# Optimization experiments

Measured on AMD Instinct MI355X. Metric: run time of the kernel, lower is better.

The kernel has to match this reference:

```python
import jax, jax.numpy as jnp
from jax import lax
import numpy as np

B, A, T = 128, 32, 32
HID = 64
DEG = 7
MODES = 25
OUT_FRAMES = 12
NHEAD, DHEAD = 16, 64


def legendre_tmat(out_frames, degree):
    # normalized Legendre basis evaluated at t_n, shape [degree+1, len(t_n)]
    t = np.arange(-6, out_frames + 1, dtype=np.float32)
    t = t / t[-1]
    P = [np.ones_like(t), t]
    for n in range(1, degree):
        P.append(((2 * n + 1) * t * P[n] - n * P[n - 1]) / (n + 1))
    P = np.stack(P[: degree + 1], 0)
    norm = np.sqrt((2 * np.arange(degree + 1) + 1) / 2.0).astype(np.float32)
    return (P * norm[:, None]).astype(np.float32)


def _conv(x, w, stride, pad):
    return lax.conv_general_dilated(x, w, (stride, stride), [(pad, pad), (pad, pad)],
                                    dimension_numbers=("NCHW", "OIHW", "NCHW"))


def _bn(x, g, b, eps=1e-5):
    m = jnp.mean(x, axis=(0, 2, 3), keepdims=True)
    v = jnp.var(x, axis=(0, 2, 3), keepdims=True)
    return (x - m) / jnp.sqrt(v + eps) * g[None, :, None, None] + b[None, :, None, None]


def setup_inputs() -> dict:
    key = jax.random.key(0)
    ks = jax.random.split(key, 32)

    def rn(i, shape, scale=0.05):
        return jax.random.normal(ks[i], shape, dtype=jnp.float32) * scale

    inp = {
        "cnn_feat": rn(0, (B, 1024, 14, 14), 1.0),
        "ego_state": rn(1, (B, T, 5), 1.0),
        "agents_state": rn(2, (B, A, T, 5), 1.0),
        "ego_state_len": jax.random.randint(ks[3], (B,), 0, T),
        "agents_state_len": jax.random.randint(ks[4], (B, A), 0, T),
        "agents_grid_pos": jax.random.randint(ks[5], (B, A, 2), 0, 14),
        "state_fc_W": rn(6, (HID, 5)), "state_fc_b": rn(7, (HID,)),
        "lstm_Wih": rn(8, (4 * HID, HID)), "lstm_Whh": rn(9, (4 * HID, HID)),
        "lstm_bih": rn(10, (4 * HID,)), "lstm_bhh": rn(11, (4 * HID,)),
        "enc_fc_W": rn(12, (HID, HID)), "enc_fc_b": rn(13, (HID,)),
        "conv1_W": rn(14, (512, 1024 + HID, 3, 3)),
        "bn1_g": jnp.ones((512,), jnp.float32), "bn1_b": jnp.zeros((512,), jnp.float32),
        "conv2_W": rn(15, (512, 512, 3, 3)),
        "bn2_g": jnp.ones((512,), jnp.float32), "bn2_b": jnp.zeros((512,), jnp.float32),
        "q_W": rn(16, (NHEAD * DHEAD, 512 + HID)),
        "k_W": rn(17, (NHEAD * DHEAD, 512, 1, 1)),
        "v_W": rn(18, (NHEAD * DHEAD, 512, 1, 1)),
        "attn_out_W": rn(19, (512, NHEAD * DHEAD)), "attn_out_b": rn(20, (512,)),
        "cls_W": rn(21, (MODES, 512 + HID + 512)), "cls_b": rn(22, (MODES,)),
        "dec1_W": rn(23, (256, 512 + HID + 512)), "dec1_b": rn(24, (256,)),
        "dec2_W": rn(25, ((DEG + 1) * 2 * MODES, 256)), "dec2_b": rn(26, ((DEG + 1) * 2 * MODES,)),
    }
    return inp


def reference(cnn_feat, ego_state, agents_state, ego_state_len, agents_state_len,
              agents_grid_pos, state_fc_W, state_fc_b, lstm_Wih, lstm_Whh, lstm_bih,
              lstm_bhh, enc_fc_W, enc_fc_b, conv1_W, bn1_g, bn1_b, conv2_W, bn2_g,
              bn2_b, q_W, k_W, v_W, attn_out_W, attn_out_b, cls_W, cls_b, dec1_W,
              dec1_b, dec2_W, dec2_b):
    Bn, _, Hs, Ws = cnn_feat.shape

    def lstm_encode(seq, lens):
        # seq [N,T,5]; packed-sequence semantics with zero init == take h at step len-1
        N, Tn, _ = seq.shape
        h = seq @ state_fc_W.T + state_fc_b  # [N,T,64]

        def step(carry, xt):
            hh, cc = carry
            g = xt @ lstm_Wih.T + hh @ lstm_Whh.T + lstm_bih + lstm_bhh
            i, f_, gg, o = jnp.split(g, 4, axis=-1)
            cc = jax.nn.sigmoid(f_) * cc + jax.nn.sigmoid(i) * jnp.tanh(gg)
            hh = jax.nn.sigmoid(o) * jnp.tanh(cc)
            return (hh, cc), hh

        z = jnp.zeros((N, HID), h.dtype)
        _, hs = lax.scan(step, (z, z), h.transpose(1, 0, 2))  # hs [T,N,64]
        idx = jnp.clip(lens, 1, Tn).astype(jnp.int32) - 1
        last = hs[idx, jnp.arange(N)]
        return last @ enc_fc_W.T + enc_fc_b

    ego = lstm_encode(ego_state, ego_state_len)  # [B,64]
    ag = lstm_encode(agents_state.reshape(Bn * A, T, 5),
                     agents_state_len.reshape(-1)).reshape(Bn, A, HID)

    # scatter-add agent encodings into the spatial grid (overlapping writes accumulate)
    grid = jnp.zeros((Bn, Hs, Ws, HID), cnn_feat.dtype)
    bidx = jnp.broadcast_to(jnp.arange(Bn)[:, None], (Bn, A))
    grid = grid.at[bidx, agents_grid_pos[..., 0], agents_grid_pos[..., 1]].add(ag)

    x = jnp.concatenate([cnn_feat, grid.transpose(0, 3, 1, 2)], axis=1)
    x = jax.nn.relu(_bn(_conv(x, conv1_W, 1, 1), bn1_g, bn1_b))
    x = jax.nn.relu(_bn(_conv(x, conv2_W, 2, 1), bn2_g, bn2_b))  # [B,512,7,7]

    ego_t = jnp.concatenate([x[:, :, 3, 3], ego], axis=1)  # [B,576]
    q = (ego_t @ q_W.T).reshape(Bn, NHEAD, DHEAD)
    k = _conv(x, k_W, 1, 1).reshape(Bn, NHEAD, DHEAD, -1)  # g = 9*9 = 81
    v = _conv(x, v_W, 1, 1).reshape(Bn, NHEAD, DHEAD, -1)
    energy = jnp.einsum("bhf,bhfg->bhg", q, k)
    attn = jax.nn.softmax(energy / (NHEAD * DHEAD) ** 0.5, axis=2)
    o = jnp.einsum("bhg,bhdg->bhd", attn, v).reshape(Bn, -1)
    o = o @ attn_out_W.T + attn_out_b

    feat = jnp.concatenate([o, ego_t], axis=1)  # [B,1088]
    conf = feat @ cls_W.T + cls_b
    d = jax.nn.relu(feat @ dec1_W.T + dec1_b)
    d = (d @ dec2_W.T + dec2_b).reshape(Bn, MODES, -1)

    tmat = jnp.asarray(legendre_tmat(OUT_FRAMES, DEG))  # [DEG+1, 19]
    out_x = d[:, :, : DEG + 1] @ tmat
    out_y = d[:, :, DEG + 1:] @ tmat
    traj = jnp.stack([out_x, out_y], axis=3)  # [B,MODES,19,2]
    return traj, conf
```

## Files before the change

kernel.cpp:

```cpp
#include <hip/hip_runtime.h>
#include <stdint.h>
#include <stddef.h>

#define DEVINL static __device__ __forceinline__

typedef __attribute__((ext_vector_type(8))) short  bfrag;
typedef __attribute__((ext_vector_type(4))) float  facc;

DEVINL uint16_t f2b(float f){
  uint32_t u = __float_as_uint(f);
  return (uint16_t)((u + 0x7fffu + ((u >> 16) & 1u)) >> 16);
}
DEVINL float b2f(uint16_t b){ return __uint_as_float(((uint32_t)b) << 16); }

DEVINL facc MFMA(bfrag a, bfrag b, facc c){
  return __builtin_amdgcn_mfma_f32_16x16x32_bf16(a, b, c, 0, 0, 0);
}

DEVINL void gload16(const void* g, void* l){
  __builtin_amdgcn_global_load_lds(
      (const __attribute__((address_space(1))) uint32_t*)g,
      (__attribute__((address_space(3))) uint32_t*)l, 16, 0, 0);
}

DEVINL float fast_tanh(float x){
  return 2.f/(1.f+__expf(-2.f*x)) - 1.f;
}

struct F2BJobs {
  const float* s[6];
  uint16_t*    d[6];
  int          n[6];
};
__global__ void k_f2b_multi(F2BJobs jobs){
  int j = blockIdx.y;
  const float* s = jobs.s[j];
  uint16_t* d = jobs.d[j];
  int n = jobs.n[j];
  int i = blockIdx.x*256 + threadIdx.x;
  int st = gridDim.x*256;
  for(; i<n; i+=st) d[i] = f2b(s[i]);
}

__global__ void k_zborder(uint16_t* __restrict__ X, uint16_t* __restrict__ Y,
                          float* __restrict__ gridb){
  int b = blockIdx.x & 127, t = threadIdx.x;
  uint16_t* base = (blockIdx.x < 128) ? X : Y;
  int C = (blockIdx.x < 128) ? 1088 : 512;
  for(int p=0;p<60;p++){
    int y, x;
    if(p<16){ y=0; x=p; }
    else if(p<32){ y=15; x=p-16; }
    else { int q=p-32; y=1+(q>>1); x=(q&1)?15:0; }
    uint32_t* dst = (uint32_t*)(base + ((size_t)(b*16+y)*16 + x)*C);
    for(int i=t;i<C/2;i+=256) dst[i] = 0;
  }
  float* g = gridb + (size_t)blockIdx.x*6272;
  for(int i=t;i<6272;i+=256) g[i] = 0.f;
}

__global__ void k_lstm_prep(const float* __restrict__ Wih, const float* __restrict__ Whh,
                            const float* __restrict__ bih, const float* __restrict__ bhh,
                            const float* __restrict__ sW, const float* __restrict__ sb,
                            const float* __restrict__ encW,
                            uint16_t* __restrict__ Wc, float* __restrict__ be,
                            uint16_t* __restrict__ encWb, float* __restrict__ tm){
  int n = threadIdx.x;
  if(n < 19){
    float tv = (float)(n - 6) / 12.0f;
    float Pm = 1.0f, Pc = tv;
    tm[0*19+n] = Pm * sqrtf(0.5f);
    tm[1*19+n] = Pc * sqrtf(1.5f);
    for(int q=1; q<7; q++){
      float Pn = ((float)(2*q+1)*tv*Pc - (float)q*Pm) / (float)(q+1);
      Pm = Pc; Pc = Pn;
      tm[(q+1)*19+n] = Pc * sqrtf((float)(2*(q+1)+1) * 0.5f);
    }
  }
  for(int k=0;k<64;k++) Wc[n*96+k] = f2b(Whh[n*64+k]);
  for(int k5=0;k5<5;k5++){
    float s = 0.f;
    for(int j=0;j<64;j++) s += Wih[n*64+j]*sW[j*5+k5];
    Wc[n*96+64+k5] = f2b(s);
  }
  for(int k=69;k<96;k++) Wc[n*96+k] = 0;
  float s = 0.f;
  for(int j=0;j<64;j++) s += Wih[n*64+j]*sb[j];
  be[n] = s + bih[n] + bhh[n];
  if(n < 64){
    for(int k=0;k<64;k++) encWb[n*64+k] = f2b(encW[n*64+k]);
  }
}

__global__ __launch_bounds__(256) void k_lstm(
    const float* __restrict__ ego_seq, const float* __restrict__ ag_seq,
    const int* __restrict__ ego_len, const int* __restrict__ ag_len,
    const int* __restrict__ grid_pos,
    const uint16_t* __restrict__ Wc, const float* __restrict__ be,
    const uint16_t* __restrict__ encWb, const float* __restrict__ encB,
    float* __restrict__ agrid, uint16_t* __restrict__ egoT, uint16_t* __restrict__ feat)
{
  __shared__ __align__(16) uint16_t A[32*96];
  __shared__ float Xf[32*160];
  __shared__ int   idxs[32];

  int t = threadIdx.x, w = t>>6, l = t&63;
  int blk = blockIdx.x;
  bool isEgo = blk < 4;
  int seq0 = isEgo ? blk*32 : (blk-4)*32;
  const float* seqp = (isEgo ? ego_seq : ag_seq) + (size_t)seq0*160;

  for(int i=t;i<32*160;i+=256) Xf[i] = seqp[i];
  if(t < 32){
    int L = isEgo ? ego_len[seq0+t] : ag_len[seq0+t];
    if(L < 1) L = 1;
    idxs[t] = L-1;
  }
  for(int i=t;i<32*96;i+=256) A[i] = 0;

  bfrag bf[4][3];
  float be4[4];
  for(int ct=0;ct<4;ct++){
    int n = (ct*4+w)*16 + (l&15);
    for(int ks=0;ks<3;ks++)
      bf[ct][ks] = *(const bfrag*)(Wc + n*96 + ks*32 + (l>>4)*8);
    be4[ct] = be[n];
  }
  float cst[8], hl[8];
  for(int i=0;i<8;i++){ cst[i]=0.f; hl[i]=0.f; }
  __syncthreads();
  int myidx[8];
  for(int rt=0;rt<2;rt++) for(int r=0;r<4;r++){
    int s = rt*16 + (l>>4)*4 + r;
    myidx[rt*4+r] = idxs[s];
  }

  for(int st=0; st<32; st++){
    if(t < 160){ int s=t/5, kk=t%5; A[s*96+64+kk] = f2b(Xf[s*160 + st*5 + kk]); }
    __syncthreads();
    facc acc[2][4];
    for(int rt=0;rt<2;rt++) for(int ct=0;ct<4;ct++) acc[rt][ct] = facc{0.f,0.f,0.f,0.f};
    #pragma unroll
    for(int ks=0;ks<3;ks++){
      bfrag aA[2];
      #pragma unroll
      for(int rt=0;rt<2;rt++)
        aA[rt] = *(const bfrag*)(A + (rt*16+(l&15))*96 + ks*32 + (l>>4)*8);
      #pragma unroll
      for(int rt=0;rt<2;rt++)
        #pragma unroll
        for(int ct=0;ct<4;ct++)
          acc[rt][ct] = MFMA(aA[rt], bf[ct][ks], acc[rt][ct]);
    }
    __syncthreads();
    #pragma unroll
    for(int rt=0;rt<2;rt++) for(int r=0;r<4;r++){
      int cell = rt*4+r;
      int s = rt*16 + (l>>4)*4 + r;
      float gi = acc[rt][0][r] + be4[0];
      float gf = acc[rt][1][r] + be4[1];
      float gg = acc[rt][2][r] + be4[2];
      float go = acc[rt][3][r] + be4[3];
      float si = 1.f/(1.f+__expf(-gi));
      float sf = 1.f/(1.f+__expf(-gf));
      float so = 1.f/(1.f+__expf(-go));
      float tg = fast_tanh(gg);
      float c2 = sf*cst[cell] + si*tg;
      cst[cell] = c2;
      float hn = so*fast_tanh(c2);
      A[s*96 + w*16 + (l&15)] = f2b(hn);
      if(st == myidx[cell]) hl[cell] = hn;
    }
  }
  __syncthreads();
  for(int rt=0;rt<2;rt++) for(int r=0;r<4;r++){
    int s = rt*16 + (l>>4)*4 + r;
    A[s*96 + w*16 + (l&15)] = f2b(hl[rt*4+r]);
  }
  __syncthreads();
  bfrag eb[2];
  for(int ks=0;ks<2;ks++)
    eb[ks] = *(const bfrag*)(encWb + (w*16+(l&15))*64 + ks*32 + (l>>4)*8);
  facc ea[2]; ea[0] = facc{0.f,0.f,0.f,0.f}; ea[1] = facc{0.f,0.f,0.f,0.f};
  for(int ks=0;ks<2;ks++){
    for(int rt=0;rt<2;rt++){
      bfrag aA = *(const bfrag*)(A + (rt*16+(l&15))*96 + ks*32 + (l>>4)*8);
      ea[rt] = MFMA(aA, eb[ks], ea[rt]);
    }
  }
  int n = w*16 + (l&15);
  float bn_ = encB[n];
  for(int rt=0;rt<2;rt++) for(int r=0;r<4;r++){
    int s = rt*16 + (l>>4)*4 + r;
    float v = ea[rt][r] + bn_;
    int gs = seq0 + s;
    if(isEgo){
      egoT[(size_t)gs*576 + 512 + n] = f2b(v);
      feat[(size_t)gs*1088 + 1024 + n] = f2b(v);
    } else {
      int py = grid_pos[gs*2+0], px = grid_pos[gs*2+1];
      atomicAdd(&agrid[((size_t)(gs>>5)*196 + py*14 + px)*64 + n], v);
    }
  }
}

__global__ void k_packx(const float* __restrict__ cnn, const float* __restrict__ agrid,
                        uint16_t* __restrict__ Xp)
{
  __shared__ float tile[32*200];
  int b = blockIdx.x, ch = blockIdx.y, t = threadIdx.x;
  if(ch < 32){
    int c0 = ch*32;
    for(int i=t;i<32*196;i+=256){
      int ci = i/196, s = i%196;
      tile[ci*200+s] = cnn[((size_t)b*1024 + c0+ci)*196 + s];
    }
    __syncthreads();
    for(int i=t;i<16*196;i+=256){
      int s = i>>4, c2 = i&15;
      int y = s/14, x = s%14;
      uint32_t pu = (uint32_t)f2b(tile[(2*c2)*200+s]) |
                    ((uint32_t)f2b(tile[(2*c2+1)*200+s])<<16);
      *(uint32_t*)(Xp + (((size_t)b*16 + y+1)*16 + x+1)*1088 + c0 + 2*c2) = pu;
    }
  } else {
    int j0 = (ch-32)*32;
    for(int i=t;i<16*196;i+=256){
      int s = i>>4, j2 = i&15;
      int y = s/14, x = s%14;
      const float* gsrc = agrid + ((size_t)b*196 + s)*64 + j0 + 2*j2;
      uint32_t pu = (uint32_t)f2b(gsrc[0]) | ((uint32_t)f2b(gsrc[1])<<16);
      *(uint32_t*)(Xp + (((size_t)b*16 + y+1)*16 + x+1)*1088 + 1024 + j0 + 2*j2) = pu;
    }
  }
}

__global__ void k_packw(const float* __restrict__ W, uint16_t* __restrict__ Wp, int O, int C)
{
  int o = blockIdx.x;
  int c = blockIdx.y*64 + threadIdx.x;
  const float* src = W + ((size_t)o*C + c)*9;
  float v[9];
  #pragma unroll
  for(int d=0;d<9;d++) v[d] = src[d];
  #pragma unroll
  for(int d=0;d<9;d++)
    Wp[((size_t)d*O + o)*C + c] = f2b(v[d]);
}

__global__ void k_packw2(const float* __restrict__ W, uint16_t* __restrict__ Wp)
{
  int o = blockIdx.x;
  int c = blockIdx.y*64 + threadIdx.x;
  const float* src = W + ((size_t)o*512 + c)*9;
  float v[9];
  #pragma unroll
  for(int d=0;d<9;d++) v[d] = src[d];
  #pragma unroll
  for(int dy=0;dy<3;dy++)
    #pragma unroll
    for(int dx=0;dx<3;dx++)
      Wp[((size_t)(dy*512 + o))*1536 + dx*512 + c] = f2b(v[dy*3+dx]);
}

__global__ void k_packwk(const float* __restrict__ kW, uint16_t* __restrict__ WKT)
{
  int h = blockIdx.x;
  int c0 = blockIdx.y*32;
  int t = threadIdx.x;
  int d = t & 63;
  for(int ci = t>>6; ci<32; ci+=4){
    int c = c0 + ci;
    WKT[((size_t)h*512 + c)*64 + d] = f2b(kW[((size_t)(h*64+d))*512 + c]);
  }
}

__global__ __launch_bounds__(512) void k_conv1_8p(
    const uint16_t* __restrict__ Ain, const uint16_t* __restrict__ Wb,
    uint16_t* __restrict__ Out, float* __restrict__ stats)
{
  constexpr int CB = 1088;
  constexpr int NSTEP = 153;
  __shared__ __align__(16) char LDSb[131072];

  int t = threadIdx.x, w = t>>6, l = t&63;
  int wm = w>>2, wn = w&3;

  int xcd = blockIdx.x & 7, pos = blockIdx.x >> 3;
  int wgid = (xcd < 4 ? xcd*25 : 100 + (xcd-4)*24) + pos;
  int m0 = (wgid % 98) * 256;
  int n0 = (wgid / 98) * 256;

  const uint16_t* aP[2][2];
  const uint16_t* bP[2][2];
  #pragma unroll
  for(int P=0;P<2;P++)
    #pragma unroll
    for(int j=0;j<2;j++){
      int partrow = j*64 + (t>>3);
      int swz = ((t&7) ^ (partrow&7))*8;
      int gr = P*64 + partrow + ((partrow>=64)?64:0);
      int m = m0 + gr; int b = m/196, s = m%196, y = s/14, x = s%14;
      aP[P][j] = Ain + ((b*16+y)*16+x)*CB + swz;
      int nb = n0 + (partrow>>5)*64 + P*32 + (partrow&31);
      bP[P][j] = Wb + (size_t)nb*CB + swz;
    }

  facc acc[8][4];
  #pragma unroll
  for(int i=0;i<8;i++)
    #pragma unroll
    for(int j=0;j<4;j++) acc[i][j] = facc{0.f,0.f,0.f,0.f};

  bfrag aF[4][2], bF0[2][2], bF1[2][2];
  int dd = 0;

  #define STG(buf, PART) do{                                                   \
    if((PART)==0 || (PART)==3){ const int P_ = ((PART)==3);                    \
      _Pragma("unroll")                                                        \
      for(int j_=0;j_<2;j_++)                                                  \
        gload16(aP[P_][j_], LDSb + (buf)*65536 + P_*16384 + j_*8192 + w*1024); \
    } else { const int P_ = ((PART)==2);                                       \
      _Pragma("unroll")                                                        \
      for(int j_=0;j_<2;j_++)                                                  \
        gload16(bP[P_][j_], LDSb + (buf)*65536 + 32768 + P_*16384 + j_*8192 + w*1024); \
    }                                                                          \
  }while(0)

  #define ADVK() do{                                                          \
    if(dd==8){                                                                \
      _Pragma("unroll")                                                       \
      for(int P_=0;P_<2;P_++) for(int j_=0;j_<2;j_++){                        \
        aP[P_][j_] += 64 - 34*CB; bP[P_][j_] += 64 - 8*512*CB; }              \
      dd = 0;                                                                 \
    } else {                                                                  \
      int sA_ = (dd==2||dd==5) ? 14*CB : CB;                                  \
      _Pragma("unroll")                                                       \
      for(int P_=0;P_<2;P_++) for(int j_=0;j_<2;j_++){                        \
        aP[P_][j_] += sA_; bP[P_][j_] += 512*CB; }                            \
      dd++;                                                                   \
    }                                                                         \
  }while(0)

  #define VM4 asm volatile("s_waitcnt vmcnt(4)" ::: "memory")
  #define VM2 asm volatile("s_waitcnt vmcnt(2)" ::: "memory")
  #define VM0 asm volatile("s_waitcnt vmcnt(0)" ::: "memory")

  #define LDA(mh) do{                                                         \
    const uint16_t* Ab_ = (const uint16_t*)(LDSb + p*65536 + (mh)*16384);     \
    _Pragma("unroll")                                                         \
    for(int i_=0;i_<4;i_++)                                                   \
      _Pragma("unroll")                                                       \
      for(int ks_=0;ks_<2;ks_++)                                              \
        aF[i_][ks_] = *(const bfrag*)(Ab_ + (wm*64 + i_*16 + (l&15))*64       \
                        + ((ks_*32 + (l>>4)*8) ^ ((l&7)<<3)));                \
  }while(0)

  #define LDB(dst, nh) do{                                                   \
    const uint16_t* Bb_ = (const uint16_t*)(LDSb + p*65536 + 32768 + (nh)*16384); \
    _Pragma("unroll")                                                         \
    for(int j_=0;j_<2;j_++)                                                   \
      _Pragma("unroll")                                                       \
      for(int ks_=0;ks_<2;ks_++)                                              \
        dst[j_][ks_] = *(const bfrag*)(Bb_ + (wn*32 + j_*16 + (l&15))*64      \
                        + ((ks_*32 + (l>>4)*8) ^ ((l&7)<<3)));                \
  }while(0)

  #define MM(mh, nh, bsrc) do{                                               \
    __builtin_amdgcn_s_setprio(1);                                           \
    _Pragma("unroll")                                                        \
    for(int ks_=0;ks_<2;ks_++)                                               \
      _Pragma("unroll")                                                      \
      for(int i_=0;i_<4;i_++)                                                \
        _Pragma("unroll")                                                    \
        for(int j_=0;j_<2;j_++)                                              \
          acc[(mh)*4+i_][(nh)*2+j_] =                                        \
            MFMA(aF[i_][ks_], bsrc[j_][ks_], acc[(mh)*4+i_][(nh)*2+j_]);     \
    __builtin_amdgcn_s_setprio(0);                                           \
  }while(0)

  #define BARS do{ __builtin_amdgcn_sched_barrier(0); __builtin_amdgcn_s_barrier(); }while(0)
  #define EBAR __builtin_amdgcn_s_barrier()

  STG(0,0); STG(0,1); STG(0,2); STG(0,3);
  ADVK();
  VM4;
  EBAR;

  for(int kt=0; kt<NSTEP-1; kt++){
    int p = kt&1;
    LDA(0); LDB(bF0,0); STG(p^1,0); BARS; MM(0,0,bF0); VM4; EBAR;
    LDB(bF1,1);         STG(p^1,1); BARS; MM(0,1,bF1); VM4; EBAR;
    LDA(1);             STG(p^1,2); BARS; MM(1,1,bF1);      EBAR;
                        STG(p^1,3); BARS; MM(1,0,bF0); VM4; EBAR;
    if(kt < NSTEP-2) ADVK();
  }
  {
    int p = 0;
    LDA(0); LDB(bF0,0); BARS; MM(0,0,bF0); VM2; EBAR;
    LDB(bF1,1);         BARS; MM(0,1,bF1); VM0; EBAR;
    LDA(1);             BARS; MM(1,1,bF1);      EBAR;
                        BARS; MM(1,0,bF0);      EBAR;
  }

  #undef LDA
  #undef LDB
  #undef MM
  #undef BARS
  #undef EBAR
  #undef STG
  #undef ADVK

  __syncthreads();
  int* oo = (int*)LDSb;
  if(t < 256){
    int m = m0 + t; int b = m/196, s = m%196, y = s/14, x = s%14;
    oo[t] = ((b*16 + y+1)*16 + (x+1))*512;
  }
  __syncthreads();
  #pragma unroll
  for(int i=0;i<8;i++)
    #pragma unroll
    for(int j=0;j<4;j++){
      int n = n0 + wn*64 + j*16 + (l&15);
      #pragma unroll
      for(int r=0;r<4;r++){
        int mr = wm*128 + i*16 + (l>>4)*4 + r;
        Out[(size_t)oo[mr] + n] = f2b(acc[i][j][r]);
      }
    }
  __syncthreads();
  float* sred = (float*)LDSb;
  int rg = wm*4 + (l>>4);
  #pragma unroll
  for(int j=0;j<4;j++){
    float s=0.f, q=0.f;
    #pragma unroll
    for(int i=0;i<8;i++)
      #pragma unroll
      for(int r=0;r<4;r++){ float v = acc[i][j][r]; s += v; q += v*v; }
    int nl = wn*64 + j*16 + (l&15);
    sred[(nl*8 + rg)*2+0] = s;
    sred[(nl*8 + rg)*2+1] = q;
  }
  __syncthreads();
  if(t < 256){
    float s=0.f, q=0.f;
    #pragma unroll
    for(int rgi=0;rgi<8;rgi++){ s += sred[(t*8+rgi)*2]; q += sred[(t*8+rgi)*2+1]; }
    atomicAdd(&stats[n0+t], s);
    atomicAdd(&stats[512+n0+t], q);
  }
}

__global__ __launch_bounds__(256) void k_conv2dy(
    const uint16_t* __restrict__ Ain, const uint16_t* __restrict__ Wb,
    uint16_t* __restrict__ PS)
{
  __shared__ __align__(16) uint16_t As[128*64];
  __shared__ __align__(16) uint16_t Bs[128*64];

  int t = threadIdx.x, w = t>>6, l = t&63;
  int dy = blockIdx.y;

  int xcd = blockIdx.x & 7, pos = blockIdx.x >> 3;
  int wgid = (xcd < 4 ? xcd*25 : 100 + (xcd-4)*24) + pos;
  int n0 = (wgid / 49) * 128;
  int m0 = (wgid % 49) * 128;

  const uint16_t* aP[4];
  const uint16_t* bP[4];
  #pragma unroll
  for(int p=0;p<4;p++){
    int r = w*32 + p*8 + (l>>3);
    int m = m0 + r;
    int b = m/49, s = m%49, y = s/7, x = s%7;
    aP[p] = Ain + ((b*16 + 2*y + dy)*16 + 2*x)*512 + (l&7)*8;
    bP[p] = Wb + ((size_t)(dy*512 + n0 + r))*1536 + (l&7)*8;
  }

  facc acc[4][4];
  #pragma unroll
  for(int i=0;i<4;i++)
    #pragma unroll
    for(int j=0;j<4;j++) acc[i][j] = facc{0.f,0.f,0.f,0.f};
  int wm = w>>1, wn = w&1;
  char* asDst = (char*)As + w*4096;
  char* bsDst = (char*)Bs + w*4096;

  for(int stp=0; stp<24; stp++){
    #pragma unroll
    for(int p=0;p<4;p++){ gload16(aP[p], asDst + p*1024); aP[p] += 64; }
    #pragma unroll
    for(int p=0;p<4;p++){ gload16(bP[p], bsDst + p*1024); bP[p] += 64; }
    __syncthreads();
    #pragma unroll
    for(int ks=0;ks<2;ks++){
      bfrag a[4], b[4];
      #pragma unroll
      for(int i=0;i<4;i++)
        a[i] = *(const bfrag*)(As + (wm*64 + i*16 + (l&15))*64 + ks*32 + (l>>4)*8);
      #pragma unroll
      for(int j=0;j<4;j++)
        b[j] = *(const bfrag*)(Bs + (wn*64 + j*16 + (l&15))*64 + ks*32 + (l>>4)*8);
      #pragma unroll
      for(int i=0;i<4;i++)
        #pragma unroll
        for(int j=0;j<4;j++)
          acc[i][j] = MFMA(a[i], b[j], acc[i][j]);
    }
    __syncthreads();
  }

  uint16_t* out = PS + (size_t)dy*3211264;
  #pragma unroll
  for(int i=0;i<4;i++)
    #pragma unroll
    for(int j=0;j<4;j++){
      int n = n0 + wn*64 + j*16 + (l&15);
      #pragma unroll
      for(int r=0;r<4;r++){
        int mr = m0 + wm*64 + i*16 + (l>>4)*4 + r;
        out[(size_t)mr*512 + n] = f2b(acc[i][j][r]);
      }
    }
}

__global__ void k_bn2sum(const uint16_t* __restrict__ PS, uint16_t* __restrict__ Y2,
                         float* __restrict__ stats)
{
  int t = threadIdx.x;
  int m0 = blockIdx.x*16;
  float s0=0,s1=0,q0=0,q1=0;
  for(int i=0;i<16;i++){
    size_t off = (size_t)(m0+i)*512 + 2*t;
    uint32_t u0 = *(const uint32_t*)(PS + off);
    uint32_t u1 = *(const uint32_t*)(PS + 3211264 + off);
    uint32_t u2 = *(const uint32_t*)(PS + 6422528 + off);
    float a = b2f((uint16_t)u0)+b2f((uint16_t)u1)+b2f((uint16_t)u2);
    float c = b2f((uint16_t)(u0>>16))+b2f((uint16_t)(u1>>16))+b2f((uint16_t)(u2>>16));
    s0+=a; q0+=a*a; s1+=c; q1+=c*c;
    *(uint32_t*)(Y2 + off) = (uint32_t)f2b(a) | ((uint32_t)f2b(c)<<16);
  }
  atomicAdd(&stats[2*t],   s0);
  atomicAdd(&stats[2*t+1], s1);
  atomicAdd(&stats[512+2*t],   q0);
  atomicAdd(&stats[512+2*t+1], q1);
}

template<int PAD>
__global__ void k_bnapply(uint16_t* __restrict__ Y, const float* __restrict__ stats,
                          const float* __restrict__ gg, const float* __restrict__ bb,
                          int M, float invM,
                          uint16_t* __restrict__ egoT, uint16_t* __restrict__ feat)
{
  int t = threadIdx.x;
  int m0 = blockIdx.x*8;
  float mu0 = stats[2*t]*invM,       mu1 = stats[2*t+1]*invM;
  float v0 = stats[512+2*t]*invM - mu0*mu0, v1 = stats[512+2*t+1]*invM - mu1*mu1;
  float sc0 = gg[2*t]  *rsqrtf(v0+1e-5f), sc1 = gg[2*t+1]*rsqrtf(v1+1e-5f);
  float sh0 = bb[2*t]   - mu0*sc0,        sh1 = bb[2*t+1] - mu1*sc1;
  for(int i=0;i<8;i++){
    int m = m0+i; if(m>=M) break;
    size_t off;
    if(PAD){ int b=m/196, s=m%196, y=s/14, x=s%14; off = (((size_t)b*16+y+1)*16 + x+1)*512; }
    else off = (size_t)m*512;
    uint32_t u = *(const uint32_t*)(Y + off + 2*t);
    float a = fmaxf(b2f((uint16_t)u)*sc0 + sh0, 0.f);
    float c = fmaxf(b2f((uint16_t)(u>>16))*sc1 + sh1, 0.f);
    uint32_t pu = (uint32_t)f2b(a) | ((uint32_t)f2b(c)<<16);
    *(uint32_t*)(Y + off + 2*t) = pu;
    if(!PAD && (m%49)==24){
      int b = m/49;
      *(uint32_t*)(egoT + (size_t)b*576 + 2*t) = pu;
      *(uint32_t*)(feat + (size_t)b*1088 + 512 + 2*t) = pu;
    }
  }
}

__global__ __launch_bounds__(256) void k_sgemm(
    const uint16_t* __restrict__ A, int lda,
    const uint16_t* __restrict__ B, int ldb,
    const float* __restrict__ bias,
    void* __restrict__ C, int ldc,
    int N, int K, int flags)
{
  int t = threadIdx.x, w = t>>6, l = t&63;
  int nt = blockIdx.x*4 + w;
  int n  = nt*16 + (l&15);
  int m0 = blockIdx.y*16;
  bool nv = n < N;
  facc acc = facc{0.f,0.f,0.f,0.f};
  for(int k=0;k<K;k+=32){
    bfrag af = *(const bfrag*)(A + (size_t)(m0+(l&15))*lda + k + (l>>4)*8);
    bfrag bf_ = {0,0,0,0,0,0,0,0};
    if(nv) bf_ = *(const bfrag*)(B + (size_t)n*ldb + k + (l>>4)*8);
    acc = MFMA(af, bf_, acc);
  }
  if(nv){
    float bv = bias ? bias[n] : 0.f;
    #pragma unroll
    for(int r=0;r<4;r++){
      int m = m0 + (l>>4)*4 + r;
      float v = acc[r] + bv;
      if(flags & 1) v = fmaxf(v, 0.f);
      if(flags & 2) ((float*)C)[(size_t)m*ldc + n] = v;
      else ((uint16_t*)C)[(size_t)m*ldc + n] = f2b(v);
    }
  }
}

__global__ __launch_bounds__(256) void k_bgemm(
    const uint16_t* __restrict__ A, int lda, int aoffs,
    const uint16_t* __restrict__ B, int ldb, int brows,
    uint16_t* __restrict__ C, int ldc, int coffs,
    int K)
{
  int t = threadIdx.x, w = t>>6, l = t&63;
  int z = blockIdx.z;
  int n = (blockIdx.x*4 + w)*16 + (l&15);
  int m0 = blockIdx.y*16;
  const uint16_t* Ab = A + (size_t)z*aoffs;
  const uint16_t* Bb = B + (size_t)z*brows*ldb;
  facc acc = facc{0.f,0.f,0.f,0.f};
  for(int k=0;k<K;k+=32){
    bfrag af = *(const bfrag*)(Ab + (size_t)(m0+(l&15))*lda + k + (l>>4)*8);
    bfrag bf_ = *(const bfrag*)(Bb + (size_t)n*ldb + k + (l>>4)*8);
    acc = MFMA(af, bf_, acc);
  }
  #pragma unroll
  for(int r=0;r<4;r++){
    int m = m0 + (l>>4)*4 + r;
    C[(size_t)m*ldc + z*coffs + n] = f2b(acc[r]);
  }
}

__global__ __launch_bounds__(512) void k_attn2(
    const uint16_t* __restrict__ U16, const uint16_t* __restrict__ y2,
    uint16_t* __restrict__ zout)
{
  __shared__ __align__(16) char LA[49*1024 + 8*1024];
  uint16_t* uls = (uint16_t*)(LA + 49*1024);
  int t = threadIdx.x, w = t>>6, l = t&63;
  int b = blockIdx.x >> 1, half = blockIdx.x & 1;
  int h = half*8 + w;

  for(int i=t; i<3136; i+=512){
    int g = i>>6, c16 = i&63;
    *(uint4*)(LA + g*1024 + ((c16*16) ^ ((g&31)<<4))) =
        *(const uint4*)(y2 + ((size_t)(b*49+g)*512 + c16*8));
  }
  *(uint4*)((char*)uls + w*1024 + l*16) =
      *(const uint4*)(U16 + (size_t)b*8192 + h*512 + l*8);
  __syncthreads();

  float dot = 0.f;
  if(l < 49){
    const char* yrow = LA + l*1024;
    const char* ur = (const char*)uls + w*1024;
    for(int c16=0;c16<64;c16++){
      uint4 uv = *(const uint4*)(ur + c16*16);
      uint4 yv = *(const uint4*)(yrow + ((c16*16) ^ ((l&31)<<4)));
      const uint16_t* up = (const uint16_t*)&uv;
      const uint16_t* yp = (const uint16_t*)&yv;
      #pragma unroll
      for(int j=0;j<8;j++) dot += b2f(up[j])*b2f(yp[j]);
    }
  }
  float e = (l<49) ? dot*(1.f/32.f) : -1e30f;
  float mx = e;
  for(int s=32;s>0;s>>=1) mx = fmaxf(mx, __shfl_xor(mx, s));
  mx = fmaxf(mx, 0.f);
  float p = (l<49) ? __expf(e-mx) : 0.f;
  float den = p;
  for(int s=32;s>0;s>>=1) den += __shfl_xor(den, s);
  den += 32.f*__expf(-mx);

  float z[8];
  #pragma unroll
  for(int j=0;j<8;j++) z[j]=0.f;
  for(int g=0; g<49; g++){
    float pg = __shfl(p, g);
    uint4 yv = *(const uint4*)(LA + g*1024 + ((l*16) ^ ((g&31)<<4)));
    const uint16_t* yp = (const uint16_t*)&yv;
    #pragma unroll
    for(int j=0;j<8;j++) z[j] += pg*b2f(yp[j]);
  }
  float inv = 1.f/den;
  uint16_t zr[8];
  #pragma unroll
  for(int j=0;j<8;j++) zr[j] = f2b(z[j]*inv);
  *(uint4*)(zout + ((size_t)(b*16+h)*512) + l*8) = *(uint4*)zr;
}

__global__ void k_traj(const float* __restrict__ d2, const float* __restrict__ tm,
                       float* __restrict__ out)
{
  int i = blockIdx.x*256 + threadIdx.x;
  if(i >= 3200) return;
  const float* dp = d2 + (size_t)i*16;
  float cx[8], cy[8];
  #pragma unroll
  for(int j=0;j<8;j++){ cx[j]=dp[j]; cy[j]=dp[8+j]; }
  float* op = out + (size_t)i*38;
  for(int tt=0;tt<19;tt++){
    float x=0.f, y=0.f;
    #pragma unroll
    for(int j=0;j<8;j++){ float tv = tm[j*19+tt]; x += cx[j]*tv; y += cy[j]*tv; }
    op[tt*2+0]=x; op[tt*2+1]=y;
  }
}

extern "C" void kernel_launch(void* const* d_in, const int* in_sizes, int n_in,
                              void* d_out, int out_size, void* d_ws, size_t ws_size,
                              hipStream_t stream)
{
  const float* cnn      = (const float*)d_in[0];
  const float* ego_seq  = (const float*)d_in[1];
  const float* ag_seq   = (const float*)d_in[2];
  const int*   ego_len  = (const int*)d_in[3];
  const int*   ag_len   = (const int*)d_in[4];
  const int*   grid_pos = (const int*)d_in[5];
  const float* sW  = (const float*)d_in[6];
  const float* sb  = (const float*)d_in[7];
  const float* Wih = (const float*)d_in[8];
  const float* Whh = (const float*)d_in[9];
  const float* bih = (const float*)d_in[10];
  const float* bhh = (const float*)d_in[11];
  const float* encW = (const float*)d_in[12];
  const float* encB = (const float*)d_in[13];
  const float* conv1W = (const float*)d_in[14];
  const float* bn1g = (const float*)d_in[15];
  const float* bn1b = (const float*)d_in[16];
  const float* conv2W = (const float*)d_in[17];
  const float* bn2g = (const float*)d_in[18];
  const float* bn2b = (const float*)d_in[19];
  const float* qWf  = (const float*)d_in[20];
  const float* kWf  = (const float*)d_in[21];
  const float* vWf  = (const float*)d_in[22];
  const float* aoW  = (const float*)d_in[23];
  const float* aoB  = (const float*)d_in[24];
  const float* clsWf = (const float*)d_in[25];
  const float* clsB  = (const float*)d_in[26];
  const float* d1Wf  = (const float*)d_in[27];
  const float* d1B   = (const float*)d_in[28];
  const float* d2Wf  = (const float*)d_in[29];
  const float* d2B   = (const float*)d_in[30];

  char* ws = (char*)d_ws;
  const size_t XP_OFF   = 0;
  const size_t PS_OFF   = 0;
  const size_t U_OFF    = 0;
  const size_t ZB_OFF   = 2097152;
  const size_t Y2_OFF   = 41943040;
  const size_t Y1P_OFF  = 71303168;
  const size_t WP1_OFF  = 104857600;
  const size_t WP2_OFF  = 114884608;
  const size_t WKT_OFF  = 119603200;
  const size_t WVB_OFF  = 120651776;
  const size_t QW_OFF   = 121700352;
  const size_t AOW_OFF  = 122880000;
  const size_t CLSW_OFF = 123928576;
  const size_t D1W_OFF  = 123982976;
  const size_t D2W_OFF  = 124540032;
  const size_t GRID_OFF = 124744832;
  const size_t EGOT_OFF = 131167360;
  const size_t FEAT_OFF = 131314816;
  const size_t QB_OFF   = 131593344;
  const size_t OBUF_OFF = 132117632;
  const size_t D1_OFF   = 132379776;
  const size_t D2_OFF   = 132445312;
  const size_t WC_OFF   = 132650112;
  const size_t BE_OFF   = 132699264;
  const size_t ENCW_OFF = 132700288;
  const size_t TMAT_OFF = 132708480;
  const size_t ST1_OFF  = 132709120;
  const size_t ST2_OFF  = 132713216;

  uint16_t* XP   = (uint16_t*)(ws + XP_OFF);
  uint16_t* PSB  = (uint16_t*)(ws + PS_OFF);
  uint16_t* U16  = (uint16_t*)(ws + U_OFF);
  uint16_t* ZB16 = (uint16_t*)(ws + ZB_OFF);
  uint16_t* Y2   = (uint16_t*)(ws + Y2_OFF);
  uint16_t* Y1P  = (uint16_t*)(ws + Y1P_OFF);
  uint16_t* WP1  = (uint16_t*)(ws + WP1_OFF);
  uint16_t* WP2  = (uint16_t*)(ws + WP2_OFF);
  uint16_t* WKT  = (uint16_t*)(ws + WKT_OFF);
  uint16_t* WVB  = (uint16_t*)(ws + WVB_OFF);
  uint16_t* QW   = (uint16_t*)(ws + QW_OFF);
  uint16_t* AOW  = (uint16_t*)(ws + AOW_OFF);
  uint16_t* CLSW = (uint16_t*)(ws + CLSW_OFF);
  uint16_t* D1W  = (uint16_t*)(ws + D1W_OFF);
  uint16_t* D2W  = (uint16_t*)(ws + D2W_OFF);
  float*    GRIDB= (float*)(ws + GRID_OFF);
  uint16_t* EGOT = (uint16_t*)(ws + EGOT_OFF);
  uint16_t* FEAT = (uint16_t*)(ws + FEAT_OFF);
  uint16_t* QB16 = (uint16_t*)(ws + QB_OFF);
  uint16_t* OBUF = (uint16_t*)(ws + OBUF_OFF);
  uint16_t* D1B  = (uint16_t*)(ws + D1_OFF);
  float*    D2B  = (float*)(ws + D2_OFF);
  uint16_t* WC   = (uint16_t*)(ws + WC_OFF);
  float*    BE   = (float*)(ws + BE_OFF);
  uint16_t* ENCWB= (uint16_t*)(ws + ENCW_OFF);
  float*    TMAT = (float*)(ws + TMAT_OFF);
  float*    ST1  = (float*)(ws + ST1_OFF);
  float*    ST2  = (float*)(ws + ST2_OFF);
  float*    outF = (float*)d_out;

  (void)hipMemsetAsync(ws + ST1_OFF,  0, 8192, stream);

  k_zborder<<<256,256,0,stream>>>(XP, Y1P, GRIDB);

  k_lstm_prep<<<1,256,0,stream>>>(Wih,Whh,bih,bhh,sW,sb,encW, WC,BE,ENCWB, TMAT);
  k_packw<<<dim3(512,17),64,0,stream>>>(conv1W, WP1, 512, 1088);
  k_packw2<<<dim3(512,8),64,0,stream>>>(conv2W, WP2);
  k_packwk<<<dim3(16,16),256,0,stream>>>(kWf, WKT);
  {
    F2BJobs jb;
    jb.s[0]=vWf;  jb.d[0]=WVB;   jb.n[0]=1024*512;
    jb.s[1]=qWf;  jb.d[1]=QW;    jb.n[1]=1024*576;
    jb.s[2]=aoW;  jb.d[2]=AOW;   jb.n[2]=512*1024;
    jb.s[3]=clsWf;jb.d[3]=CLSW;  jb.n[3]=25*1088;
    jb.s[4]=d1Wf; jb.d[4]=D1W;   jb.n[4]=256*1088;
    jb.s[5]=d2Wf; jb.d[5]=D2W;   jb.n[5]=400*256;
    k_f2b_multi<<<dim3(48,6),256,0,stream>>>(jb);
  }

  k_lstm<<<132,256,0,stream>>>(ego_seq, ag_seq, ego_len, ag_len, grid_pos,
                               WC, BE, ENCWB, encB, GRIDB, EGOT, FEAT);
  k_packx<<<dim3(128,34),256,0,stream>>>(cnn, GRIDB, XP);
  k_conv1_8p<<<196,512,0,stream>>>(XP, WP1, Y1P, ST1);
  k_bnapply<1><<<3136,256,0,stream>>>(Y1P, ST1, bn1g, bn1b, 25088, 1.f/25088.f, nullptr, nullptr);
  k_conv2dy<<<dim3(196,3),256,0,stream>>>(Y1P, WP2, PSB);
  k_bn2sum<<<392,256,0,stream>>>(PSB, Y2, ST2);
  k_bnapply<0><<<784,256,0,stream>>>(Y2, ST2, bn2g, bn2b, 6272, 1.f/6272.f, EGOT, FEAT);
  k_sgemm<<<dim3(16,8),256,0,stream>>>(EGOT, 576, QW, 576, nullptr, QB16, 1024, 1024, 576, 0);
  k_bgemm<<<dim3(8,8,16),256,0,stream>>>(QB16, 1024, 64, WKT, 64, 512, U16, 8192, 512, 64);
  k_attn2<<<256,512,0,stream>>>(U16, Y2, ZB16);
  k_bgemm<<<dim3(1,8,16),256,0,stream>>>(ZB16, 8192, 512, WVB, 512, 64, OBUF, 1024, 64, 512);
  k_sgemm<<<dim3(8,8),256,0,stream>>>(OBUF, 1024, AOW, 1024, aoB, FEAT, 1088, 512, 1024, 0);
  k_sgemm<<<dim3(1,8),256,0,stream>>>(FEAT, 1088, CLSW, 1088, clsB, outF + 121600, 25, 25, 1088, 2);
  k_sgemm<<<dim3(4,8),256,0,stream>>>(FEAT, 1088, D1W, 1088, d1B, D1B, 256, 256, 1088, 1);
  k_sgemm<<<dim3(7,8),256,0,stream>>>(D1B, 256, D2W, 256, d2B, D2B, 400, 400, 256, 2);
  k_traj<<<13,256,0,stream>>>(D2B, TMAT, outF);

  (void)in_sizes; (void)n_in; (void)out_size; (void)ws_size;
}
```

Before: 596.3 us.

## Double-buffer conv2 LDS loads and fuse tail GEMM launches and stats memset

The conv2 GEMM kernel gets double-buffered LDS staging. The next K-step's global-to-LDS loads are issued before computing on the current buffer, using explicit vmcnt waits and barriers. This is meant to hide load latency behind MFMA work, at the cost of twice the shared memory, which may lower occupancy. The BN stats memset is folded into the border-zeroing kernel, and the classifier and dec1 GEMMs are merged into one launch to cut launch overhead.

```diff
diff --git a/kernel.cpp b/kernel.cpp
--- a/kernel.cpp
+++ b/kernel.cpp
@@ -43,7 +43,7 @@
 }
 
 __global__ void k_zborder(uint16_t* __restrict__ X, uint16_t* __restrict__ Y,
-                          float* __restrict__ gridb){
+                          float* __restrict__ gridb, float* __restrict__ stats){
   int b = blockIdx.x & 127, t = threadIdx.x;
   uint16_t* base = (blockIdx.x < 128) ? X : Y;
   int C = (blockIdx.x < 128) ? 1088 : 512;
@@ -57,6 +57,9 @@
   }
   float* g = gridb + (size_t)blockIdx.x*6272;
   for(int i=t;i<6272;i+=256) g[i] = 0.f;
+  if(blockIdx.x == 0){
+    for(int i=t;i<2048;i+=256) stats[i] = 0.f;
+  }
 }
 
 __global__ void k_lstm_prep(const float* __restrict__ Wih, const float* __restrict__ Whh,
@@ -457,8 +460,8 @@
     const uint16_t* __restrict__ Ain, const uint16_t* __restrict__ Wb,
     uint16_t* __restrict__ PS)
 {
-  __shared__ __align__(16) uint16_t As[128*64];
-  __shared__ __align__(16) uint16_t Bs[128*64];
+  __shared__ __align__(16) uint16_t As[2*128*64];
+  __shared__ __align__(16) uint16_t Bs[2*128*64];
 
   int t = threadIdx.x, w = t>>6, l = t&63;
   int dy = blockIdx.y;
@@ -485,32 +488,54 @@
     #pragma unroll
     for(int j=0;j<4;j++) acc[i][j] = facc{0.f,0.f,0.f,0.f};
   int wm = w>>1, wn = w&1;
-  char* asDst = (char*)As + w*4096;
-  char* bsDst = (char*)Bs + w*4096;
-
-  for(int stp=0; stp<24; stp++){
-    #pragma unroll
-    for(int p=0;p<4;p++){ gload16(aP[p], asDst + p*1024); aP[p] += 64; }
-    #pragma unroll
-    for(int p=0;p<4;p++){ gload16(bP[p], bsDst + p*1024); bP[p] += 64; }
-    __syncthreads();
-    #pragma unroll
-    for(int ks=0;ks<2;ks++){
-      bfrag a[4], b[4];
-      #pragma unroll
-      for(int i=0;i<4;i++)
-        a[i] = *(const bfrag*)(As + (wm*64 + i*16 + (l&15))*64 + ks*32 + (l>>4)*8);
-      #pragma unroll
-      for(int j=0;j<4;j++)
-        b[j] = *(const bfrag*)(Bs + (wn*64 + j*16 + (l&15))*64 + ks*32 + (l>>4)*8);
-      #pragma unroll
-      for(int i=0;i<4;i++)
-        #pragma unroll
-        for(int j=0;j<4;j++)
-          acc[i][j] = MFMA(a[i], b[j], acc[i][j]);
-    }
-    __syncthreads();
-  }
+
+  #define C2STG(buf) do{                                                    \
+    char* ad_ = (char*)As + (buf)*16384 + w*4096;                           \
+    char* bd_ = (char*)Bs + (buf)*16384 + w*4096;                           \
+    _Pragma("unroll")                                                       \
+    for(int p=0;p<4;p++){ gload16(aP[p], ad_ + p*1024); aP[p] += 64; }      \
+    _Pragma("unroll")                                                       \
+    for(int p=0;p<4;p++){ gload16(bP[p], bd_ + p*1024); bP[p] += 64; }      \
+  }while(0)
+
+  #define C2CMP(buf) do{                                                    \
+    const uint16_t* Ab_ = As + (buf)*8192;                                  \
+    const uint16_t* Bb_ = Bs + (buf)*8192;                                  \
+    _Pragma("unroll")                                                       \
+    for(int ks=0;ks<2;ks++){                                                \
+      bfrag a_[4], b_[4];                                                   \
+      _Pragma("unroll")                                                     \
+      for(int i=0;i<4;i++)                                                  \
+        a_[i] = *(const bfrag*)(Ab_ + (wm*64 + i*16 + (l&15))*64 + ks*32 + (l>>4)*8); \
+      _Pragma("unroll")                                                     \
+      for(int j=0;j<4;j++)                                                  \
+        b_[j] = *(const bfrag*)(Bb_ + (wn*64 + j*16 + (l&15))*64 + ks*32 + (l>>4)*8); \
+      _Pragma("unroll")                                                     \
+      for(int i=0;i<4;i++)                                                  \
+        _Pragma("unroll")                                                   \
+        for(int j=0;j<4;j++)                                                \
+          acc[i][j] = MFMA(a_[i], b_[j], acc[i][j]);                        \
+    }                                                                       \
+  }while(0)
+
+  C2STG(0);
+  asm volatile("s_waitcnt vmcnt(0)" ::: "memory");
+  __builtin_amdgcn_s_barrier();
+  for(int stp=0; stp<23; stp++){
+    C2STG((stp+1)&1);
+    asm volatile("s_waitcnt vmcnt(8)" ::: "memory");
+    __builtin_amdgcn_sched_barrier(0);
+    __builtin_amdgcn_s_barrier();
+    C2CMP(stp&1);
+    __builtin_amdgcn_sched_barrier(0);
+    __builtin_amdgcn_s_barrier();
+  }
+  asm volatile("s_waitcnt vmcnt(0)" ::: "memory");
+  __builtin_amdgcn_s_barrier();
+  C2CMP(1);
+
+  #undef C2STG
+  #undef C2CMP
 
   uint16_t* out = PS + (size_t)dy*3211264;
   #pragma unroll
@@ -606,6 +631,39 @@
       if(flags & 1) v = fmaxf(v, 0.f);
       if(flags & 2) ((float*)C)[(size_t)m*ldc + n] = v;
       else ((uint16_t*)C)[(size_t)m*ldc + n] = f2b(v);
+    }
+  }
+}
+
+__global__ __launch_bounds__(256) void k_tail1(
+    const uint16_t* __restrict__ FEAT,
+    const uint16_t* __restrict__ D1W, const float* __restrict__ d1B,
+    const uint16_t* __restrict__ CLSW, const float* __restrict__ clsB,
+    uint16_t* __restrict__ D1out, float* __restrict__ confOut)
+{
+  int t = threadIdx.x, w = t>>6, l = t&63;
+  int m0 = blockIdx.y*16;
+  bool isCls = (blockIdx.x == 4);
+  int n = (isCls ? w : (blockIdx.x*4 + w))*16 + (l&15);
+  int N = isCls ? 25 : 256;
+  const uint16_t* B = isCls ? CLSW : D1W;
+  bool nv = n < N;
+  facc acc = facc{0.f,0.f,0.f,0.f};
+  for(int k=0;k<1088;k+=32){
+    bfrag af = *(const bfrag*)(FEAT + (size_t)(m0+(l&15))*1088 + k + (l>>4)*8);
+    bfrag bf_ = {0,0,0,0,0,0,0,0};
+    if(nv) bf_ = *(const bfrag*)(B + (size_t)n*1088 + k + (l>>4)*8);
+    acc = MFMA(af, bf_, acc);
+  }
+  if(nv){
+    #pragma unroll
+    for(int r=0;r<4;r++){
+      int m = m0 + (l>>4)*4 + r;
+      if(isCls){
+        confOut[(size_t)m*25 + n] = acc[r] + clsB[n];
+      } else {
+        D1out[(size_t)m*256 + n] = f2b(fmaxf(acc[r] + d1B[n], 0.f));
+      }
     }
   }
 }
@@ -807,9 +865,7 @@
   float*    ST2  = (float*)(ws + ST2_OFF);
   float*    outF = (float*)d_out;
 
-  (void)hipMemsetAsync(ws + ST1_OFF,  0, 8192, stream);
-
-  k_zborder<<<256,256,0,stream>>>(XP, Y1P, GRIDB);
+  k_zborder<<<256,256,0,stream>>>(XP, Y1P, GRIDB, ST1);
 
   k_lstm_prep<<<1,256,0,stream>>>(Wih,Whh,bih,bhh,sW,sb,encW, WC,BE,ENCWB, TMAT);
   k_packw<<<dim3(512,17),64,0,stream>>>(conv1W, WP1, 512, 1088);
@@ -839,8 +895,7 @@
   k_attn2<<<256,512,0,stream>>>(U16, Y2, ZB16);
   k_bgemm<<<dim3(1,8,16),256,0,stream>>>(ZB16, 8192, 512, WVB, 512, 64, OBUF, 1024, 64, 512);
   k_sgemm<<<dim3(8,8),256,0,stream>>>(OBUF, 1024, AOW, 1024, aoB, FEAT, 1088, 512, 1024, 0);
-  k_sgemm<<<dim3(1,8),256,0,stream>>>(FEAT, 1088, CLSW, 1088, clsB, outF + 121600, 25, 25, 1088, 2);
-  k_sgemm<<<dim3(4,8),256,0,stream>>>(FEAT, 1088, D1W, 1088, d1B, D1B, 256, 256, 1088, 1);
+  k_tail1<<<dim3(5,8),256,0,stream>>>(FEAT, D1W, d1B, CLSW, clsB, D1B, outF + 121600);
   k_sgemm<<<dim3(7,8),256,0,stream>>>(D1B, 256, D2W, 256, d2B, D2B, 400, 400, 256, 2);
   k_traj<<<13,256,0,stream>>>(D2B, TMAT, outF);
 
```

Result: no change. 588.6 us (-1.3%).
